# Performance work log

Measured on AMD Instinct MI355X. Metric: run time of the kernel, lower is better.

## Reference

```python
import jax, jax.numpy as jnp
import numpy as np

B, C_IN, H, W = 8, 64, 128, 128
NUM_POINT = 128
N_INST = 512
INIT_STRIDE, COARSE_STRIDE, DOWN_SAMPLE = 10.0, 4.0, 4.0
D_MODEL, N_HEADS = 256, 8


def conv2d(x, w, b, pad):
    y = jax.lax.conv_general_dilated(x, w, (1, 1), [(pad, pad), (pad, pad)],
                                     dimension_numbers=('NCHW', 'OIHW', 'NCHW'))
    return y + b[None, :, None, None]


def trans_feature(x, w1, b1, w2, b2):
    # Conv3x3 -> ReLU -> Conv1x1 (c_in -> 256 -> 254)
    return conv2d(jax.nn.relu(conv2d(x, w1, b1, 1)), w2, b2, 0)


def grid_sample_points(feat, img_idx, pts):
    # get_gcn_feature: per-instance bilinear sampling of feat[img_idx] at pixel
    # coords pts. torch grid_sample(align_corners=False, padding_mode='zeros');
    # the normalize->unnormalize of pixel coords collapses to a -0.5 shift.
    Bf, C, Hf, Wf = feat.shape
    ix = pts[..., 0] - 0.5
    iy = pts[..., 1] - 0.5
    x0 = jnp.floor(ix)
    y0 = jnp.floor(iy)
    wx = ix - x0
    wy = iy - y0

    def gather(yy, xx, wgt):
        valid = (xx >= 0) & (xx < Wf) & (yy >= 0) & (yy < Hf)
        xc = jnp.clip(xx, 0, Wf - 1).astype(jnp.int32)
        yc = jnp.clip(yy, 0, Hf - 1).astype(jnp.int32)
        v = feat[img_idx[:, None], :, yc, xc]  # [N,P,C]
        return v * (wgt * valid)[..., None]

    return (gather(y0, x0, (1 - wx) * (1 - wy)) + gather(y0, x0 + 1, wx * (1 - wy))
            + gather(y0 + 1, x0, (1 - wx) * wy) + gather(y0 + 1, x0 + 1, wx * wy))


def normalize_poly(poly):
    # Center each contour and scale by its max extent -> positional encoding in [-1,1]
    mean = poly.mean(axis=1, keepdims=True)
    p = poly - mean
    scale = jnp.max(jnp.abs(p), axis=(1, 2), keepdims=True) + 1e-6
    return p / scale


def csa(x, wqkv, bqkv, wo, bo, whead, bhead):
    # ContourSelfAttention: MHSA over contour points + linear head to 2D offsets
    N, P, C = x.shape
    d = C // N_HEADS
    qkv = x @ wqkv + bqkv
    q, k, v = jnp.split(qkv, 3, axis=-1)
    sh = lambda t: t.reshape(N, P, N_HEADS, d).transpose(0, 2, 1, 3)
    q, k, v = sh(q), sh(k), sh(v)
    attn = jax.nn.softmax(jnp.einsum('nhpd,nhqd->nhpq', q, k) / jnp.sqrt(jnp.float32(d)), axis=-1)
    o = jnp.einsum('nhpq,nhqd->nhpd', attn, v).transpose(0, 2, 1, 3).reshape(N, P, C)
    o = o @ wo + bo
    return o @ whead + bhead  # [N,P,2]


def setup_inputs():
    key = jax.random.key(0)
    ks = jax.random.split(key, 32)
    s = 0.05
    inp = {
        'cnn_feature': jax.random.normal(ks[0], (B, C_IN, H, W), jnp.float32),
        'wh_pred': jax.random.normal(ks[1], (B, 2 * NUM_POINT, H, W), jnp.float32),
        'ct_ind': jax.random.randint(ks[2], (N_INST,), 0, H * W),
        'ct_img_idx': jax.random.randint(ks[3], (N_INST,), 0, B),
    }
    p = lambda i, shape: jax.random.normal(ks[i], shape, jnp.float32) * s
    for pre, i0 in (('f1', 4), ('f2', 8)):
        inp[pre + '_w1'] = p(i0, (256, C_IN, 3, 3))
        inp[pre + '_b1'] = p(i0 + 1, (256,))
        inp[pre + '_w2'] = p(i0 + 2, (254, 256, 1, 1))
        inp[pre + '_b2'] = p(i0 + 3, (254,))
    for pre, i0 in (('csa1', 12), ('csa2', 18)):
        inp[pre + '_wqkv'] = p(i0, (D_MODEL, 3 * D_MODEL))
        inp[pre + '_bqkv'] = p(i0 + 1, (3 * D_MODEL,))
        inp[pre + '_wo'] = p(i0 + 2, (D_MODEL, D_MODEL))
        inp[pre + '_bo'] = p(i0 + 3, (D_MODEL,))
        inp[pre + '_whead'] = p(i0 + 4, (D_MODEL, 2))
        inp[pre + '_bhead'] = p(i0 + 5, (2,))
    return inp


def reference(cnn_feature, wh_pred, ct_ind, ct_img_idx,
              f1_w1, f1_b1, f1_w2, f1_b2, f2_w1, f2_b1, f2_w2, f2_b2,
              csa1_wqkv, csa1_bqkv, csa1_wo, csa1_bo, csa1_whead, csa1_bhead,
              csa2_wqkv, csa2_bqkv, csa2_wo, csa2_bo, csa2_whead, csa2_bhead):
    # ---- Decode.train_decode ----
    ct_x = ct_ind % W
    ct_y = ct_ind // W
    # per-instance gather of contour offsets: wh_pred[img, :, y, x] -> [N, 2*P]
    ct_offset = wh_pred[ct_img_idx, :, ct_y, ct_x].reshape(-1, NUM_POINT, 2)
    ct = jnp.stack([ct_x, ct_y], axis=1).astype(jnp.float32)  # [N,2]
    init_polys = ct_offset * INIT_STRIDE + ct[:, None, :]     # [N,128,2]
    # ---- Refine ----
    feat1 = trans_feature(cnn_feature, f1_w1, f1_b1, f1_w2, f1_b2)  # [B,254,H,W]
    feat2 = trans_feature(cnn_feature, f2_w1, f2_b1, f2_w2, f2_b2)
    points = jnp.concatenate([ct[:, None, :], init_polys], axis=1)  # [N,129,2]
    fp1 = grid_sample_points(feat1, ct_img_idx, points)             # [N,129,254]
    x1 = jnp.concatenate([fp1, normalize_poly(points)], axis=-1)    # [N,129,256]
    offsets1 = csa(x1, csa1_wqkv, csa1_bqkv, csa1_wo, csa1_bo, csa1_whead, csa1_bhead)[:, 1:, :]
    coarse_polys = offsets1 * COARSE_STRIDE + jax.lax.stop_gradient(init_polys)
    fp2 = grid_sample_points(feat2, ct_img_idx, coarse_polys)       # [N,128,254]
    x2 = jnp.concatenate([fp2, normalize_poly(coarse_polys)], axis=-1)
    offsets2 = csa(x2, csa2_wqkv, csa2_bqkv, csa2_wo, csa2_bo, csa2_whead, csa2_bhead)
    final_polys = offsets2 + jax.lax.stop_gradient(coarse_polys)
    return (init_polys * DOWN_SAMPLE, coarse_polys * DOWN_SAMPLE, final_polys * DOWN_SAMPLE)
```

## Files before the change

### kernel.cpp

```cpp
#include <hip/hip_runtime.h>
#include <hip/hip_bf16.h>

typedef unsigned short u16;
typedef unsigned int   u32;
typedef float  f32x4 __attribute__((ext_vector_type(4)));
typedef short  s16x8 __attribute__((ext_vector_type(8)));

__device__ __forceinline__ float bf2f(u16 u) {
    return __uint_as_float(((unsigned int)u) << 16);
}
__device__ __forceinline__ u16 f2bf(float f) {
    unsigned int x = __float_as_uint(f);
    unsigned int r = x + 0x7fffu + ((x >> 16) & 1u);
    return (u16)(r >> 16);
}

#define WIMG 128
#define HIMG 128
#define PADW 130
#define BIMG 8
#define CIN  64
#define NPOINT 128
#define NINST 512

#define AS1 __attribute__((address_space(1)))
#define AS3 __attribute__((address_space(3)))
__device__ __forceinline__ void async16(const void* g, void* l) {
    __builtin_amdgcn_global_load_lds((const AS1 void*)g, (AS3 void*)l, 16, 0, 0);
}


__global__ __launch_bounds__(256) void k_cvt_w1(const float* __restrict__ w,
                                                u16* __restrict__ wb) {
    int idx = blockIdx.x * 256 + threadIdx.x;
    int oc = idx / 576, r = idx % 576;
    int kp = r >> 6, ic = r & 63;
    wb[idx] = f2bf(w[oc * 576 + ic * 9 + kp]);
}

__global__ __launch_bounds__(256) void k_cvt_w2(const float* __restrict__ w,
                                                u16* __restrict__ wb) {
    int idx = blockIdx.x * 256 + threadIdx.x;
    int oc = idx >> 8, ic = idx & 255;
    wb[idx] = (oc < 254) ? f2bf(w[oc * 256 + ic]) : (u16)0;
}

__global__ __launch_bounds__(256) void k_cvt_wqkv(const float* __restrict__ w,
                                                  u16* __restrict__ wb) {
    int idx = blockIdx.x * 256 + threadIdx.x;
    int n = idx >> 8, k = idx & 255;
    wb[idx] = f2bf(w[k * 768 + n]);
}

__global__ __launch_bounds__(256) void k_headfuse(const float* __restrict__ wo,
                                                  const float* __restrict__ bo,
                                                  const float* __restrict__ whead,
                                                  const float* __restrict__ bhead,
                                                  float* __restrict__ W2,
                                                  float* __restrict__ b2) {
    int idx = blockIdx.x * 256 + threadIdx.x;
    if (idx < 512) {
        int c = idx >> 1, j = idx & 1;
        float s = 0.f;
        for (int t = 0; t < 256; ++t)
            s = fmaf(wo[c * 256 + t], whead[t * 2 + j], s);
        W2[idx] = s;
    }
    if (idx < 2) {
        float s = bhead[idx];
        for (int t = 0; t < 256; ++t)
            s = fmaf(bo[t], whead[t * 2 + idx], s);
        b2[idx] = s;
    }
}

__global__ __launch_bounds__(256) void k_zero(u16* __restrict__ p) {
    int i = blockIdx.x * 256 + threadIdx.x;
    ((uint4*)p)[i] = make_uint4(0u, 0u, 0u, 0u);
}

__global__ __launch_bounds__(256) void k_nhwc(const float* __restrict__ in,
                                              u16* __restrict__ out) {
    __shared__ u16 sT[128][80];
    int b = blockIdx.x >> 7, y = blockIdx.x & 127;
    int tid = threadIdx.x;
    const float* ib = in + ((size_t)b * CIN * HIMG + y) * WIMG;
    int x4 = tid & 31, icg = tid >> 5;
    #pragma unroll
    for (int pass = 0; pass < 8; ++pass) {
        int ic = pass * 8 + icg;
        float4 v = *(const float4*)&ib[(size_t)ic * (HIMG * WIMG) + x4 * 4];
        sT[x4 * 4 + 0][ic] = f2bf(v.x);
        sT[x4 * 4 + 1][ic] = f2bf(v.y);
        sT[x4 * 4 + 2][ic] = f2bf(v.z);
        sT[x4 * 4 + 3][ic] = f2bf(v.w);
    }
    __syncthreads();
    u16* ob = out + ((size_t)(b * PADW + y + 1) * PADW + 1) * 64;
    int icu = tid & 7, xw = tid >> 3;
    #pragma unroll
    for (int pass = 0; pass < 4; ++pass) {
        int x = pass * 32 + xw;
        uint4 v = *(const uint4*)&sT[x][icu * 8];
        *(uint4*)&ob[(size_t)x * 64 + icu * 8] = v;
    }
}

__global__ __launch_bounds__(256) void k_init(const float* __restrict__ whp,
                                              const int* __restrict__ ct_ind,
                                              const int* __restrict__ ct_img,
                                              float* __restrict__ points1,
                                              float* __restrict__ out0) {
    int i = blockIdx.x;
    int t = threadIdx.x;
    int ind = ct_ind[i];
    int x = ind % WIMG, y = ind / WIMG;
    int b = ct_img[i];
    int p = t >> 1, c = t & 1;
    float off = whp[(((size_t)b * 2 * NPOINT + t) * HIMG + y) * WIMG + x];
    float ctc = (c == 0) ? (float)x : (float)y;
    float ip = off * 10.0f + ctc;
    points1[((size_t)i * 129 + 1 + p) * 2 + c] = ip;
    if (t < 2) points1[(size_t)i * 129 * 2 + t] = (t == 0) ? (float)x : (float)y;
    out0[((size_t)i * NPOINT + p) * 2 + c] = ip * 4.0f;
}

__global__ __launch_bounds__(256, 2) void k_convgemm(const u16* __restrict__ inTp,
                                                     const u16* __restrict__ wb1,
                                                     const float* __restrict__ b1,
                                                     const u16* __restrict__ wb2,
                                                     const float* __restrict__ b2,
                                                     u16* __restrict__ feat) {
    __shared__ u16 smem[33280];
    u16* sB = smem;
    u16* sA = smem + 16384;
    u16* sC = smem + 16384;

    int tid = threadIdx.x;
    int wave = tid >> 6, lane = tid & 63;
    int quad = lane >> 4, l16 = lane & 15;
    int rl = lane >> 2, part = lane & 3;
    int partS = part ^ ((rl ^ (rl >> 2)) & 3);
    int quadS = quad ^ ((l16 ^ (l16 >> 2)) & 3);
    int wpx = wave >> 1, woc = wave & 1;

    int bx = blockIdx.x;
    int y = (bx & 7) * 16 + (bx >> 3);
    int b = blockIdx.z;
    const u16* inb = inTp + (size_t)b * PADW * PADW * 64;

    f32x4 acc1[4][8];
    #pragma unroll
    for (int mt = 0; mt < 4; ++mt)
        #pragma unroll
        for (int nt = 0; nt < 8; ++nt)
            #pragma unroll
            for (int q = 0; q < 4; ++q) acc1[mt][nt][q] = 0.f;

    auto stageA = [&](u16* dst, int t) {
        int kp = t >> 1, ic0 = (t & 1) << 5;
        int ky = kp / 3, kx = kp - ky * 3;
        const u16* arow = inb + ((size_t)(y + ky) * PADW + kx) * 64 + ic0 + partS * 8;
        #pragma unroll
        for (int j = 0; j < 2; ++j) {
            int rr = wave * 32 + j * 16;
            async16(arow + (size_t)(rr + rl) * 64, dst + rr * 32);
        }
    };
    auto stageB1 = [&](u16* dst, int t) {
        int kp = t >> 1, ic0 = (t & 1) << 5;
        const u16* brow = wb1 + (size_t)kp * 64 + ic0 + partS * 8;
        #pragma unroll
        for (int j = 0; j < 4; ++j) {
            int rr = wave * 64 + j * 16;
            async16(brow + (size_t)(rr + rl) * 576, dst + rr * 32);
        }
    };
    auto stageB2 = [&](u16* dst, int kk) {
        #pragma unroll
        for (int j = 0; j < 4; ++j) {
            int rr = wave * 64 + j * 16;
            async16(wb2 + (size_t)(rr + rl) * 256 + kk + partS * 8, dst + rr * 32);
        }
    };

    stageA(sA, 0);
    stageB1(sB, 0);
    __syncthreads();
    int buf = 0;
    for (int t = 0; t < 18; ++t) {
        if (t < 17) {
            stageA(sA + (buf ^ 1) * 4096, t + 1);
            stageB1(sB + (buf ^ 1) * 8192, t + 1);
        }
        s16x8 aF[4], bF[8];
        #pragma unroll
        for (int mt = 0; mt < 4; ++mt)
            aF[mt] = *(const s16x8*)&sA[buf * 4096 + (wpx * 64 + mt * 16 + l16) * 32 + quadS * 8];
        #pragma unroll
        for (int nt = 0; nt < 8; ++nt)
            bF[nt] = *(const s16x8*)&sB[buf * 8192 + (woc * 128 + nt * 16 + l16) * 32 + quadS * 8];
        #pragma unroll
        for (int mt = 0; mt < 4; ++mt)
            #pragma unroll
            for (int nt = 0; nt < 8; ++nt)
                acc1[mt][nt] = __builtin_amdgcn_mfma_f32_16x16x32_bf16(
                    aF[mt], bF[nt], acc1[mt][nt], 0, 0, 0);
        __syncthreads();
        buf ^= 1;
    }

    u16* outb0 = feat + ((size_t)b * (HIMG * WIMG) + (size_t)y * 128) * 256;
    #pragma unroll 1
    for (int half = 0; half < 2; ++half) {
        if (wpx == half) {
            #pragma unroll
            for (int nt = 0; nt < 8; ++nt) {
                int col = woc * 128 + nt * 16 + l16;
                float bv = b1[col];
                #pragma unroll
                for (int mt = 0; mt < 4; ++mt) {
                    #pragma unroll
                    for (int r = 0; r < 4; ++r) {
                        int row = mt * 16 + quad * 4 + r;
                        sC[row * 264 + col] = f2bf(fmaxf(acc1[mt][nt][r] + bv, 0.f));
                    }
                }
            }
        }
        stageB2(sB, 0);
        __syncthreads();

        f32x4 acc2[4][4];
        #pragma unroll
        for (int mt = 0; mt < 4; ++mt)
            #pragma unroll
            for (int nt = 0; nt < 4; ++nt)
                #pragma unroll
                for (int q = 0; q < 4; ++q) acc2[mt][nt][q] = 0.f;
        int b2f = 0;
        for (int ik = 0; ik < 8; ++ik) {
            if (ik < 7) stageB2(sB + (b2f ^ 1) * 8192, (ik + 1) * 32);
            s16x8 a2[4], bb[4];
            #pragma unroll
            for (int mt = 0; mt < 4; ++mt)
                a2[mt] = *(const s16x8*)&sC[(mt * 16 + l16) * 264 + ik * 32 + quad * 8];
            #pragma unroll
            for (int nt = 0; nt < 4; ++nt)
                bb[nt] = *(const s16x8*)&sB[b2f * 8192 + (wave * 64 + nt * 16 + l16) * 32 + quadS * 8];
            #pragma unroll
            for (int mt = 0; mt < 4; ++mt)
                #pragma unroll
                for (int nt = 0; nt < 4; ++nt)
                    acc2[mt][nt] = __builtin_amdgcn_mfma_f32_16x16x32_bf16(
                        a2[mt], bb[nt], acc2[mt][nt], 0, 0, 0);
            __syncthreads();
            b2f ^= 1;
        }

        #pragma unroll
        for (int nt = 0; nt < 4; ++nt) {
            int col = wave * 64 + nt * 16 + l16;
            float bv = (col < 254) ? b2[col] : 0.f;
            #pragma unroll
            for (int mt = 0; mt < 4; ++mt) {
                #pragma unroll
                for (int r = 0; r < 4; ++r) {
                    int row = mt * 16 + quad * 4 + r;
                    sC[row * 264 + col] = f2bf(acc2[mt][nt][r] + bv);
                }
            }
        }
        __syncthreads();
        u16* outb = outb0 + (size_t)half * 64 * 256;
        #pragma unroll
        for (int it = 0; it < 8; ++it) {
            int idx = it * 256 + tid;
            int row = idx >> 5, ch = idx & 31;
            *(uint4*)&outb[(size_t)row * 256 + ch * 8] = *(const uint4*)&sC[row * 264 + ch * 8];
        }
        __syncthreads();
    }
}

__global__ __launch_bounds__(256, 4) void k_gemm_mfma(const u16* __restrict__ A,
                                                      const u16* __restrict__ Bt,
                                                      const float* __restrict__ bias, int nbias,
                                                      u16* __restrict__ C,
                                                      int M, int N, int K, int relu) {
    __shared__ u16 smem[16384];
    u16* sA = smem;
    u16* sB = smem + 8192;
    u16* sOut = smem;
    int tid = threadIdx.x;
    int wave = tid >> 6, lane = tid & 63;
    int quad = lane >> 4, l16 = lane & 15;
    int rl = lane >> 2, part = lane & 3;
    int partS = part ^ ((rl ^ (rl >> 2)) & 3);
    int quadS = quad ^ ((l16 ^ (l16 >> 2)) & 3);
    int r0 = wave * 32;

    int gx = gridDim.x, gy = gridDim.y;
    int o = blockIdx.y * gx + blockIdx.x;
    int nwg = gx * gy;
    int qn = nwg >> 3, r8 = nwg & 7;
    int xcd = o & 7, oi = o >> 3;
    int vid = (xcd < r8) ? xcd * (qn + 1) + oi : r8 * (qn + 1) + (xcd - r8) * qn + oi;
    int m0 = (vid / gy) * 128, n0 = (vid % gy) * 128;
    int wm = (wave >> 1) * 64, wn = (wave & 1) * 64;

    f32x4 acc[4][4];
    #pragma unroll
    for (int a = 0; a < 4; ++a)
        #pragma unroll
        for (int b = 0; b < 4; ++b)
            #pragma unroll
            for (int q = 0; q < 4; ++q) acc[a][b][q] = 0.f;

    auto stage = [&](int bufi, int kk) {
        #pragma unroll
        for (int j = 0; j < 2; ++j) {
            int rr = r0 + j * 16;
            async16(&A[(size_t)(m0 + rr + rl) * K + kk + partS * 8], &sA[bufi * 4096 + rr * 32]);
            async16(&Bt[(size_t)(n0 + rr + rl) * K + kk + partS * 8], &sB[bufi * 4096 + rr * 32]);
        }
    };

    stage(0, 0);
    __syncthreads();
    int buf = 0;
    int nk = K >> 5;
    for (int ik = 0; ik < nk; ++ik) {
        if (ik + 1 < nk) stage(buf ^ 1, (ik + 1) << 5);
        s16x8 aF[4], bF[4];
        #pragma unroll
        for (int mt = 0; mt < 4; ++mt)
            aF[mt] = *(const s16x8*)&sA[buf * 4096 + (wm + mt * 16 + l16) * 32 + quadS * 8];
        #pragma unroll
        for (int nt = 0; nt < 4; ++nt)
            bF[nt] = *(const s16x8*)&sB[buf * 4096 + (wn + nt * 16 + l16) * 32 + quadS * 8];
        #pragma unroll
        for (int mt = 0; mt < 4; ++mt)
            #pragma unroll
            for (int nt = 0; nt < 4; ++nt)
                acc[mt][nt] = __builtin_amdgcn_mfma_f32_16x16x32_bf16(
                    aF[mt], bF[nt], acc[mt][nt], 0, 0, 0);
        __syncthreads();
        buf ^= 1;
    }

    #pragma unroll
    for (int pass = 0; pass < 2; ++pass) {
        if ((wave >> 1) == pass) {
            #pragma unroll
            for (int nt = 0; nt < 4; ++nt) {
                int col = wn + nt * 16 + l16;
                int gcol = n0 + col;
                float bv = (gcol < nbias) ? bias[gcol] : 0.f;
                #pragma unroll
                for (int mt = 0; mt < 4; ++mt) {
                    #pragma unroll
                    for (int r = 0; r < 4; ++r) {
                        int rowl = mt * 16 + quad * 4 + r;
                        float v = acc[mt][nt][r] + bv;
                        if (relu) v = fmaxf(v, 0.f);
                        sOut[rowl * 132 + col] = f2bf(v);
                    }
                }
            }
        }
        __syncthreads();
        #pragma unroll
        for (int it = 0; it < 8; ++it) {
            int idx = it * 256 + tid;
            int rowl = idx >> 5, ch = idx & 31;
            *(uint2*)&C[(size_t)(m0 + pass * 64 + rowl) * N + n0 + ch * 4] =
                *(const uint2*)&sOut[rowl * 132 + ch * 4];
        }
        __syncthreads();
    }
}

__global__ __launch_bounds__(256) void k_norm(const float* __restrict__ pts,
                                              u16* __restrict__ xout, int P) {
    int i = blockIdx.x, t = threadIdx.x;
    __shared__ float sx[256], sy[256];
    float px = 0.f, py = 0.f;
    if (t < P) {
        px = pts[((size_t)i * P + t) * 2 + 0];
        py = pts[((size_t)i * P + t) * 2 + 1];
    }
    sx[t] = px; sy[t] = py;
    __syncthreads();
    for (int s = 128; s > 0; s >>= 1) {
        if (t < s) { sx[t] += sx[t + s]; sy[t] += sy[t + s]; }
        __syncthreads();
    }
    float mx = sx[0] / (float)P, my = sy[0] / (float)P;
    __syncthreads();
    float ax = 0.f;
    if (t < P) ax = fmaxf(fabsf(px - mx), fabsf(py - my));
    sx[t] = ax;
    __syncthreads();
    for (int s = 128; s > 0; s >>= 1) {
        if (t < s) sx[t] = fmaxf(sx[t], sx[t + s]);
        __syncthreads();
    }
    float scale = sx[0] + 1e-6f;
    if (t < P) {
        size_t base = ((size_t)i * P + t) * 256;
        xout[base + 254] = f2bf((px - mx) / scale);
        xout[base + 255] = f2bf((py - my) / scale);
    }
}

__global__ __launch_bounds__(256) void k_sample(const u16* __restrict__ feat,
                                                const float* __restrict__ pts,
                                                const int* __restrict__ ct_img,
                                                u16* __restrict__ xout, int P) {
    int i = blockIdx.x;
    int p = blockIdx.y * 2 + (threadIdx.x >> 7);
    int c0 = (threadIdx.x & 127) * 2;
    if (p >= P || c0 >= 254) return;
    float px = pts[((size_t)i * P + p) * 2 + 0];
    float py = pts[((size_t)i * P + p) * 2 + 1];
    int b = ct_img[i];
    float ix = px - 0.5f, iy = py - 0.5f;
    float x0f = floorf(ix), y0f = floorf(iy);
    float wx = ix - x0f, wy = iy - y0f;
    int x0 = (int)x0f, y0 = (int)y0f;
    float a0 = 0.f, a1 = 0.f;
    #pragma unroll
    for (int dy = 0; dy < 2; ++dy) {
        #pragma unroll
        for (int dx = 0; dx < 2; ++dx) {
            int xx = x0 + dx, yy = y0 + dy;
            float w = (dx ? wx : 1.f - wx) * (dy ? wy : 1.f - wy);
            if (xx >= 0 && xx < WIMG && yy >= 0 && yy < HIMG) {
                u32 v = *(const u32*)&feat[(((size_t)b * HIMG + yy) * WIMG + xx) * 256 + c0];
                a0 = fmaf(w, bf2f((u16)(v & 0xffffu)), a0);
                a1 = fmaf(w, bf2f((u16)(v >> 16)), a1);
            }
        }
    }
    u32 st = (u32)f2bf(a0) | ((u32)f2bf(a1) << 16);
    *(u32*)&xout[((size_t)i * P + p) * 256 + c0] = st;
}

__global__ __launch_bounds__(256) void k_attn_mfma(const u16* __restrict__ qkv,
                                                   u16* __restrict__ obuf,
                                                   int P) {
    __shared__ u16 smem[144 * 40 * 2 + 32 * 168];
    u16* sQ = smem;
    u16* sK = smem + 144 * 40;
    u16* sVT = smem + 2 * 144 * 40;

    int il = blockIdx.x, h = blockIdx.y;
    int tid = threadIdx.x;
    int wave = tid >> 6, lane = tid & 63;
    int quad = lane >> 4, l16 = lane & 15;

    {
        u32* z = (u32*)smem;
        for (int i = tid; i < (144 * 40 * 2 + 32 * 168) / 2; i += 256) z[i] = 0u;
    }
    __syncthreads();
    for (int idx = tid; idx < 129 * 16 && (idx >> 4) < P; idx += 256) {
        int row = idx >> 4, c2 = idx & 15;
        size_t gb = ((size_t)il * P + row) * 768 + h * 32 + c2 * 2;
        *(u32*)&sQ[row * 40 + c2 * 2] = *(const u32*)&qkv[gb];
        *(u32*)&sK[row * 40 + c2 * 2] = *(const u32*)&qkv[gb + 256];
        u32 v = *(const u32*)&qkv[gb + 512];
        int kin = row & 31;
        int pcol = (row & ~31) + ((kin >> 2) & 3) * 8 + (kin >> 4) * 4 + (kin & 3);
        int d0 = c2 * 2;
        sVT[d0 * 168 + pcol] = (u16)(v & 0xffffu);
        sVT[(d0 + 1) * 168 + pcol] = (u16)(v >> 16);
    }
    __syncthreads();

    const float scale = 0.17677669529663689f;
    for (int qt = wave; qt < 9; qt += 4) {
        s16x8 bq = *(const s16x8*)&sQ[(qt * 16 + l16) * 40 + quad * 8];
        f32x4 s4[9];
        #pragma unroll
        for (int kt = 0; kt < 9; ++kt) {
            s16x8 aK = *(const s16x8*)&sK[(kt * 16 + l16) * 40 + quad * 8];
            f32x4 zz = {0.f, 0.f, 0.f, 0.f};
            s4[kt] = __builtin_amdgcn_mfma_f32_16x16x32_bf16(aK, bq, zz, 0, 0, 0);
        }
        float mx = -1e30f;
        #pragma unroll
        for (int kt = 0; kt < 9; ++kt)
            #pragma unroll
            for (int r = 0; r < 4; ++r) {
                int k = kt * 16 + quad * 4 + r;
                float v = (k < P) ? s4[kt][r] * scale : -1e30f;
                s4[kt][r] = v;
                mx = fmaxf(mx, v);
            }
        mx = fmaxf(mx, __shfl_xor(mx, 16));
        mx = fmaxf(mx, __shfl_xor(mx, 32));
        float l = 0.f;
        #pragma unroll
        for (int kt = 0; kt < 9; ++kt)
            #pragma unroll
            for (int r = 0; r < 4; ++r) {
                float e = __expf(s4[kt][r] - mx);
                s4[kt][r] = e;
                l += e;
            }
        l += __shfl_xor(l, 16);
        l += __shfl_xor(l, 32);
        u16 pb[9][4];
        #pragma unroll
        for (int kt = 0; kt < 9; ++kt)
            #pragma unroll
            for (int r = 0; r < 4; ++r) pb[kt][r] = f2bf(s4[kt][r]);
        f32x4 o[2];
        #pragma unroll
        for (int mt = 0; mt < 2; ++mt)
            #pragma unroll
            for (int q = 0; q < 4; ++q) o[mt][q] = 0.f;
        #pragma unroll
        for (int t = 0; t < 5; ++t) {
            s16x8 bp;
            #pragma unroll
            for (int j = 0; j < 4; ++j) bp[j] = (short)pb[2 * t][j];
            #pragma unroll
            for (int j = 0; j < 4; ++j)
                bp[4 + j] = (2 * t + 1 < 9) ? (short)pb[2 * t + 1][j] : (short)0;
            #pragma unroll
            for (int mt = 0; mt < 2; ++mt) {
                s16x8 aV = *(const s16x8*)&sVT[(mt * 16 + l16) * 168 + t * 32 + quad * 8];
                o[mt] = __builtin_amdgcn_mfma_f32_16x16x32_bf16(aV, bp, o[mt], 0, 0, 0);
            }
        }
        int q = qt * 16 + l16;
        if (q < P) {
            float inv = 1.f / l;
            size_t ob = ((size_t)il * P + q) * 256 + h * 32;
            #pragma unroll
            for (int mt = 0; mt < 2; ++mt) {
                ushort4 st;
                st.x = f2bf(o[mt][0] * inv);
                st.y = f2bf(o[mt][1] * inv);
                st.z = f2bf(o[mt][2] * inv);
                st.w = f2bf(o[mt][3] * inv);
                *(ushort4*)&obuf[ob + mt * 16 + quad * 4] = st;
            }
        }
    }
}

__global__ __launch_bounds__(256) void k_head1(const u16* __restrict__ obuf,
                                               const float* __restrict__ W2,
                                               const float* __restrict__ b2,
                                               const float* __restrict__ pts1,
                                               float* __restrict__ coarse,
                                               float* __restrict__ out1) {
    int wave = threadIdx.x >> 6, lane = threadIdx.x & 63;
    int m = blockIdx.x * 4 + wave;
    const u16* orow = obuf + (size_t)m * 256;
    ushort4 u = *(const ushort4*)(orow + lane * 4);
    float4 w0 = *(const float4*)(W2 + lane * 8);
    float4 w1 = *(const float4*)(W2 + lane * 8 + 4);
    float c0 = bf2f(u.x), c1 = bf2f(u.y), c2 = bf2f(u.z), c3 = bf2f(u.w);
    float s0 = c0 * w0.x + c1 * w0.z + c2 * w1.x + c3 * w1.z;
    float s1 = c0 * w0.y + c1 * w0.w + c2 * w1.y + c3 * w1.w;
    for (int off = 32; off > 0; off >>= 1) {
        s0 += __shfl_down(s0, off);
        s1 += __shfl_down(s1, off);
    }
    if (lane == 0) {
        int i = m / 129, p = m % 129;
        if (p > 0) {
            float o0 = s0 + b2[0], o1 = s1 + b2[1];
            float i0 = pts1[(size_t)m * 2 + 0];
            float i1 = pts1[(size_t)m * 2 + 1];
            float cc0 = o0 * 4.f + i0, cc1 = o1 * 4.f + i1;
            size_t cm = (size_t)i * 128 + (p - 1);
            coarse[cm * 2 + 0] = cc0;
            coarse[cm * 2 + 1] = cc1;
            out1[cm * 2 + 0] = cc0 * 4.f;
            out1[cm * 2 + 1] = cc1 * 4.f;
        }
    }
}

__global__ __launch_bounds__(256) void k_head2(const u16* __restrict__ obuf,
                                               const float* __restrict__ W2,
                                               const float* __restrict__ b2,
                                               const float* __restrict__ coarse,
                                               float* __restrict__ out2) {
    int wave = threadIdx.x >> 6, lane = threadIdx.x & 63;
    int m = blockIdx.x * 4 + wave;
    const u16* orow = obuf + (size_t)m * 256;
    ushort4 u = *(const ushort4*)(orow + lane * 4);
    float4 w0 = *(const float4*)(W2 + lane * 8);
    float4 w1 = *(const float4*)(W2 + lane * 8 + 4);
    float c0 = bf2f(u.x), c1 = bf2f(u.y), c2 = bf2f(u.z), c3 = bf2f(u.w);
    float s0 = c0 * w0.x + c1 * w0.z + c2 * w1.x + c3 * w1.z;
    float s1 = c0 * w0.y + c1 * w0.w + c2 * w1.y + c3 * w1.w;
    for (int off = 32; off > 0; off >>= 1) {
        s0 += __shfl_down(s0, off);
        s1 += __shfl_down(s1, off);
    }
    if (lane == 0) {
        float f0 = s0 + b2[0] + coarse[(size_t)m * 2 + 0];
        float f1 = s1 + b2[1] + coarse[(size_t)m * 2 + 1];
        out2[(size_t)m * 2 + 0] = f0 * 4.f;
        out2[(size_t)m * 2 + 1] = f1 * 4.f;
    }
}

extern "C" void kernel_launch(void* const* d_in, const int* in_sizes, int n_in,
                              void* d_out, int out_size, void* d_ws, size_t ws_size,
                              hipStream_t stream) {
    const float* cnn     = (const float*)d_in[0];
    const float* whp     = (const float*)d_in[1];
    const int*   ct_ind  = (const int*)d_in[2];
    const int*   ct_img  = (const int*)d_in[3];
    const float* f1_w1   = (const float*)d_in[4];
    const float* f1_b1   = (const float*)d_in[5];
    const float* f1_w2   = (const float*)d_in[6];
    const float* f1_b2   = (const float*)d_in[7];
    const float* f2_w1   = (const float*)d_in[8];
    const float* f2_b1   = (const float*)d_in[9];
    const float* f2_w2   = (const float*)d_in[10];
    const float* f2_b2   = (const float*)d_in[11];
    const float* c1_wqkv = (const float*)d_in[12];
    const float* c1_bqkv = (const float*)d_in[13];
    const float* c1_wo   = (const float*)d_in[14];
    const float* c1_bo   = (const float*)d_in[15];
    const float* c1_wh   = (const float*)d_in[16];
    const float* c1_bh   = (const float*)d_in[17];
    const float* c2_wqkv = (const float*)d_in[18];
    const float* c2_bqkv = (const float*)d_in[19];
    const float* c2_wo   = (const float*)d_in[20];
    const float* c2_bo   = (const float*)d_in[21];
    const float* c2_wh   = (const float*)d_in[22];
    const float* c2_bh   = (const float*)d_in[23];

    char* ws = (char*)d_ws;
    float* points1 = (float*)(ws + 0);
    float* coarse  = (float*)(ws + 528384);
    float* W2_1    = (float*)(ws + 1052672);
    float* b2_1    = (float*)(ws + 1054720);
    float* W2_2    = (float*)(ws + 1054976);
    float* b2_2    = (float*)(ws + 1057024);
    u16*   wb1a    = (u16*)(ws + 1057280);
    u16*   wb1b    = (u16*)(ws + 1352192);
    u16*   wb2a    = (u16*)(ws + 1647104);
    u16*   wb2b    = (u16*)(ws + 1778176);
    u16*   wqT1    = (u16*)(ws + 1909248);
    u16*   wqT2    = (u16*)(ws + 2302464);
    u16*   inT     = (u16*)(ws + 2695680);
    u16*   feat    = (u16*)(ws + 20001280);
    u16*   xbuf    = (u16*)(ws + 87110144);
    u16*   qkv_all = (u16*)(ws + 120926720);

    float* out0 = (float*)d_out;
    float* out1 = out0 + 131072;
    float* out2 = out0 + 262144;

    k_cvt_w1<<<576, 256, 0, stream>>>(f1_w1, wb1a);
    k_cvt_w1<<<576, 256, 0, stream>>>(f2_w1, wb1b);
    k_cvt_w2<<<256, 256, 0, stream>>>(f1_w2, wb2a);
    k_cvt_w2<<<256, 256, 0, stream>>>(f2_w2, wb2b);
    k_cvt_wqkv<<<768, 256, 0, stream>>>(c1_wqkv, wqT1);
    k_cvt_wqkv<<<768, 256, 0, stream>>>(c2_wqkv, wqT2);
    k_headfuse<<<2, 256, 0, stream>>>(c1_wo, c1_bo, c1_wh, c1_bh, W2_1, b2_1);
    k_headfuse<<<2, 256, 0, stream>>>(c2_wo, c2_bo, c2_wh, c2_bh, W2_2, b2_2);
    k_init<<<NINST, 256, 0, stream>>>(whp, ct_ind, ct_img, points1, out0);
    k_zero<<<4225, 256, 0, stream>>>(inT);
    k_nhwc<<<1024, 256, 0, stream>>>(cnn, inT);

    k_convgemm<<<dim3(128, 1, 8), 256, 0, stream>>>(inT, wb1a, f1_b1, wb2a, f1_b2, feat);
    k_norm<<<NINST, 256, 0, stream>>>(points1, xbuf, 129);
    k_sample<<<dim3(NINST, 65), 256, 0, stream>>>(feat, points1, ct_img, xbuf, 129);
    k_gemm_mfma<<<dim3(516, 6), 256, 0, stream>>>(xbuf, wqT1, c1_bqkv, 768, qkv_all,
                                                  66048, 768, 256, 0);
    k_attn_mfma<<<dim3(NINST, 8), 256, 0, stream>>>(qkv_all, xbuf, 129);
    k_head1<<<16512, 256, 0, stream>>>(xbuf, W2_1, b2_1, points1, coarse, out1);

    k_convgemm<<<dim3(128, 1, 8), 256, 0, stream>>>(inT, wb1b, f2_b1, wb2b, f2_b2, feat);
    k_norm<<<NINST, 256, 0, stream>>>(coarse, xbuf, 128);
    k_sample<<<dim3(NINST, 64), 256, 0, stream>>>(feat, coarse, ct_img, xbuf, 128);
    k_gemm_mfma<<<dim3(512, 6), 256, 0, stream>>>(xbuf, wqT2, c2_bqkv, 768, qkv_all,
                                                  65536, 768, 256, 0);
    k_attn_mfma<<<dim3(NINST, 8), 256, 0, stream>>>(qkv_all, xbuf, 128);
    k_head2<<<16384, 256, 0, stream>>>(xbuf, W2_2, b2_2, coarse, out2);
}
```

Measured before the change: 856.2 us.

## Split conv-GEMM blocks into half-row tiles with a shared-memory input halo window

```diff
diff --git a/kernel.cpp b/kernel.cpp
--- a/kernel.cpp
+++ b/kernel.cpp
@@ -28,7 +28,6 @@
 __device__ __forceinline__ void async16(const void* g, void* l) {
     __builtin_amdgcn_global_load_lds((const AS1 void*)g, (AS3 void*)l, 16, 0, 0);
 }
-
 
 __global__ __launch_bounds__(256) void k_cvt_w1(const float* __restrict__ w,
                                                 u16* __restrict__ wb) {
@@ -133,7 +132,7 @@
                                                      u16* __restrict__ feat) {
     __shared__ u16 smem[33280];
     u16* sB = smem;
-    u16* sA = smem + 16384;
+    u16* sW = smem + 16384;
     u16* sC = smem + 16384;
 
     int tid = threadIdx.x;
@@ -142,31 +141,21 @@
     int rl = lane >> 2, part = lane & 3;
     int partS = part ^ ((rl ^ (rl >> 2)) & 3);
     int quadS = quad ^ ((l16 ^ (l16 >> 2)) & 3);
-    int wpx = wave >> 1, woc = wave & 1;
 
     int bx = blockIdx.x;
-    int y = (bx & 7) * 16 + (bx >> 3);
+    int y = (bx & 7) * 16 + (bx >> 4);
+    int half = (bx >> 3) & 1;
+    int xb = half * 64;
     int b = blockIdx.z;
     const u16* inb = inTp + (size_t)b * PADW * PADW * 64;
 
-    f32x4 acc1[4][8];
-    #pragma unroll
-    for (int mt = 0; mt < 4; ++mt)
-        #pragma unroll
-        for (int nt = 0; nt < 8; ++nt)
-            #pragma unroll
-            for (int q = 0; q < 4; ++q) acc1[mt][nt][q] = 0.f;
-
-    auto stageA = [&](u16* dst, int t) {
-        int kp = t >> 1, ic0 = (t & 1) << 5;
-        int ky = kp / 3, kx = kp - ky * 3;
-        const u16* arow = inb + ((size_t)(y + ky) * PADW + kx) * 64 + ic0 + partS * 8;
-        #pragma unroll
-        for (int j = 0; j < 2; ++j) {
-            int rr = wave * 32 + j * 16;
-            async16(arow + (size_t)(rr + rl) * 64, dst + rr * 32);
-        }
-    };
+    for (int idx = tid; idx < 1584; idx += 256) {
+        int r = idx / 528, g = idx - r * 528;
+        int pxw = g >> 3, c = g & 7;
+        uint4 v = *(const uint4*)&inb[((size_t)(y + r) * PADW + xb + pxw) * 64 + c * 8];
+        *(uint4*)&sW[((r * 66 + pxw) * 8 + (c ^ (pxw & 7))) * 8] = v;
+    }
+
     auto stageB1 = [&](u16* dst, int t) {
         int kp = t >> 1, ic0 = (t & 1) << 5;
         const u16* brow = wb1 + (size_t)kp * 64 + ic0 + partS * 8;
@@ -184,102 +173,104 @@
         }
     };
 
-    stageA(sA, 0);
+    f32x4 acc1[4][4];
+    #pragma unroll
+    for (int mt = 0; mt < 4; ++mt)
+        #pragma unroll
+        for (int nt = 0; nt < 4; ++nt)
+            #pragma unroll
+            for (int q = 0; q < 4; ++q) acc1[mt][nt][q] = 0.f;
+
     stageB1(sB, 0);
     __syncthreads();
     int buf = 0;
     for (int t = 0; t < 18; ++t) {
-        if (t < 17) {
-            stageA(sA + (buf ^ 1) * 4096, t + 1);
-            stageB1(sB + (buf ^ 1) * 8192, t + 1);
-        }
-        s16x8 aF[4], bF[8];
+        if (t < 17) stageB1(sB + (buf ^ 1) * 8192, t + 1);
+        int kp = t >> 1, cdb = (t & 1) << 2;
+        int ky = kp / 3, kx = kp - ky * 3;
+        s16x8 aF[4], bF[4];
+        #pragma unroll
+        for (int mt = 0; mt < 4; ++mt) {
+            int pxw = kx + mt * 16 + l16;
+            int cd = cdb + quad;
+            aF[mt] = *(const s16x8*)&sW[((ky * 66 + pxw) * 8 + (cd ^ (pxw & 7))) * 8];
+        }
+        #pragma unroll
+        for (int nt = 0; nt < 4; ++nt)
+            bF[nt] = *(const s16x8*)&sB[buf * 8192 + (wave * 64 + nt * 16 + l16) * 32 + quadS * 8];
         #pragma unroll
         for (int mt = 0; mt < 4; ++mt)
-            aF[mt] = *(const s16x8*)&sA[buf * 4096 + (wpx * 64 + mt * 16 + l16) * 32 + quadS * 8];
-        #pragma unroll
-        for (int nt = 0; nt < 8; ++nt)
-            bF[nt] = *(const s16x8*)&sB[buf * 8192 + (woc * 128 + nt * 16 + l16) * 32 + quadS * 8];
-        #pragma unroll
-        for (int mt = 0; mt < 4; ++mt)
-            #pragma unroll
-            for (int nt = 0; nt < 8; ++nt)
+            #pragma unroll
+            for (int nt = 0; nt < 4; ++nt)
                 acc1[mt][nt] = __builtin_amdgcn_mfma_f32_16x16x32_bf16(
                     aF[mt], bF[nt], acc1[mt][nt], 0, 0, 0);
         __syncthreads();
         buf ^= 1;
     }
 
-    u16* outb0 = feat + ((size_t)b * (HIMG * WIMG) + (size_t)y * 128) * 256;
-    #pragma unroll 1
-    for (int half = 0; half < 2; ++half) {
-        if (wpx == half) {
-            #pragma unroll
-            for (int nt = 0; nt < 8; ++nt) {
-                int col = woc * 128 + nt * 16 + l16;
-                float bv = b1[col];
-                #pragma unroll
-                for (int mt = 0; mt < 4; ++mt) {
-                    #pragma unroll
-                    for (int r = 0; r < 4; ++r) {
-                        int row = mt * 16 + quad * 4 + r;
-                        sC[row * 264 + col] = f2bf(fmaxf(acc1[mt][nt][r] + bv, 0.f));
-                    }
-                }
-            }
-        }
-        stageB2(sB, 0);
+    #pragma unroll
+    for (int nt = 0; nt < 4; ++nt) {
+        int col = wave * 64 + nt * 16 + l16;
+        float bv = b1[col];
+        #pragma unroll
+        for (int mt = 0; mt < 4; ++mt) {
+            #pragma unroll
+            for (int r = 0; r < 4; ++r) {
+                int row = mt * 16 + quad * 4 + r;
+                sC[row * 264 + col] = f2bf(fmaxf(acc1[mt][nt][r] + bv, 0.f));
+            }
+        }
+    }
+    stageB2(sB, 0);
+    __syncthreads();
+
+    f32x4 acc2[4][4];
+    #pragma unroll
+    for (int mt = 0; mt < 4; ++mt)
+        #pragma unroll
+        for (int nt = 0; nt < 4; ++nt)
+            #pragma unroll
+            for (int q = 0; q < 4; ++q) acc2[mt][nt][q] = 0.f;
+    int b2f = 0;
+    for (int ik = 0; ik < 8; ++ik) {
+        if (ik < 7) stageB2(sB + (b2f ^ 1) * 8192, (ik + 1) * 32);
+        s16x8 a2[4], bb[4];
+        #pragma unroll
+        for (int mt = 0; mt < 4; ++mt)
+            a2[mt] = *(const s16x8*)&sC[(mt * 16 + l16) * 264 + ik * 32 + quad * 8];
+        #pragma unroll
+        for (int nt = 0; nt < 4; ++nt)
+            bb[nt] = *(const s16x8*)&sB[b2f * 8192 + (wave * 64 + nt * 16 + l16) * 32 + quadS * 8];
+        #pragma unroll
+        for (int mt = 0; mt < 4; ++mt)
+            #pragma unroll
+            for (int nt = 0; nt < 4; ++nt)
+                acc2[mt][nt] = __builtin_amdgcn_mfma_f32_16x16x32_bf16(
+                    a2[mt], bb[nt], acc2[mt][nt], 0, 0, 0);
         __syncthreads();
-
-        f32x4 acc2[4][4];
-        #pragma unroll
-        for (int mt = 0; mt < 4; ++mt)
-            #pragma unroll
-            for (int nt = 0; nt < 4; ++nt)
-                #pragma unroll
-                for (int q = 0; q < 4; ++q) acc2[mt][nt][q] = 0.f;
-        int b2f = 0;
-        for (int ik = 0; ik < 8; ++ik) {
-            if (ik < 7) stageB2(sB + (b2f ^ 1) * 8192, (ik + 1) * 32);
-            s16x8 a2[4], bb[4];
-            #pragma unroll
-            for (int mt = 0; mt < 4; ++mt)
-                a2[mt] = *(const s16x8*)&sC[(mt * 16 + l16) * 264 + ik * 32 + quad * 8];
-            #pragma unroll
-            for (int nt = 0; nt < 4; ++nt)
-                bb[nt] = *(const s16x8*)&sB[b2f * 8192 + (wave * 64 + nt * 16 + l16) * 32 + quadS * 8];
-            #pragma unroll
-            for (int mt = 0; mt < 4; ++mt)
-                #pragma unroll
-                for (int nt = 0; nt < 4; ++nt)
-                    acc2[mt][nt] = __builtin_amdgcn_mfma_f32_16x16x32_bf16(
-                        a2[mt], bb[nt], acc2[mt][nt], 0, 0, 0);
-            __syncthreads();
-            b2f ^= 1;
-        }
-
-        #pragma unroll
-        for (int nt = 0; nt < 4; ++nt) {
-            int col = wave * 64 + nt * 16 + l16;
-            float bv = (col < 254) ? b2[col] : 0.f;
-            #pragma unroll
-            for (int mt = 0; mt < 4; ++mt) {
-                #pragma unroll
-                for (int r = 0; r < 4; ++r) {
-                    int row = mt * 16 + quad * 4 + r;
-                    sC[row * 264 + col] = f2bf(acc2[mt][nt][r] + bv);
-                }
-            }
-        }
-        __syncthreads();
-        u16* outb = outb0 + (size_t)half * 64 * 256;
-        #pragma unroll
-        for (int it = 0; it < 8; ++it) {
-            int idx = it * 256 + tid;
-            int row = idx >> 5, ch = idx & 31;
-            *(uint4*)&outb[(size_t)row * 256 + ch * 8] = *(const uint4*)&sC[row * 264 + ch * 8];
-        }
-        __syncthreads();
+        b2f ^= 1;
+    }
+
+    #pragma unroll
+    for (int nt = 0; nt < 4; ++nt) {
+        int col = wave * 64 + nt * 16 + l16;
+        float bv = (col < 254) ? b2[col] : 0.f;
+        #pragma unroll
+        for (int mt = 0; mt < 4; ++mt) {
+            #pragma unroll
+            for (int r = 0; r < 4; ++r) {
+                int row = mt * 16 + quad * 4 + r;
+                sC[row * 264 + col] = f2bf(acc2[mt][nt][r] + bv);
+            }
+        }
+    }
+    __syncthreads();
+    u16* outb = feat + ((size_t)b * (HIMG * WIMG) + (size_t)y * 128 + half * 64) * 256;
+    #pragma unroll
+    for (int it = 0; it < 8; ++it) {
+        int idx = it * 256 + tid;
+        int row = idx >> 5, ch = idx & 31;
+        *(uint4*)&outb[(size_t)row * 256 + ch * 8] = *(const uint4*)&sC[row * 264 + ch * 8];
     }
 }
 
@@ -676,7 +667,7 @@
     k_zero<<<4225, 256, 0, stream>>>(inT);
     k_nhwc<<<1024, 256, 0, stream>>>(cnn, inT);
 
-    k_convgemm<<<dim3(128, 1, 8), 256, 0, stream>>>(inT, wb1a, f1_b1, wb2a, f1_b2, feat);
+    k_convgemm<<<dim3(256, 1, 8), 256, 0, stream>>>(inT, wb1a, f1_b1, wb2a, f1_b2, feat);
     k_norm<<<NINST, 256, 0, stream>>>(points1, xbuf, 129);
     k_sample<<<dim3(NINST, 65), 256, 0, stream>>>(feat, points1, ct_img, xbuf, 129);
     k_gemm_mfma<<<dim3(516, 6), 256, 0, stream>>>(xbuf, wqT1, c1_bqkv, 768, qkv_all,
@@ -684,7 +675,7 @@
     k_attn_mfma<<<dim3(NINST, 8), 256, 0, stream>>>(qkv_all, xbuf, 129);
     k_head1<<<16512, 256, 0, stream>>>(xbuf, W2_1, b2_1, points1, coarse, out1);
 
-    k_convgemm<<<dim3(128, 1, 8), 256, 0, stream>>>(inT, wb1b, f2_b1, wb2b, f2_b2, feat);
+    k_convgemm<<<dim3(256, 1, 8), 256, 0, stream>>>(inT, wb1b, f2_b1, wb2b, f2_b2, feat);
     k_norm<<<NINST, 256, 0, stream>>>(coarse, xbuf, 128);
     k_sample<<<dim3(NINST, 64), 256, 0, stream>>>(feat, coarse, ct_img, xbuf, 128);
     k_gemm_mfma<<<dim3(512, 6), 256, 0, stream>>>(xbuf, wqT2, c2_bqkv, 768, qkv_all,
```

New measurement: 755.5 us. 1.13x faster.
